# Optimization experiments

Measured on AMD Instinct MI355X. Metric: run time of the kernel, lower is better.

Reference implementation:

```python
import jax, jax.numpy as jnp
import numpy as np
import math

# Fixed rendering constants (from module-level source)
FOV_X = 60.0
FOV_Y = 60.0
NEAR = 0.1
FAR = 10000.0
SCALE_MODIFIER = 1.0
MAX_FREQUENCY = 128.0
NUM_TOTAL_FREQUENCIES = 1024
GAUSSIAN_ONLY = False
COV_DILATION = 0.3  # low-pass dilation as in 3DGS EWA splatting

N_PRIM = 512
TOP_K = 8
IMG_H = 200
IMG_W = 200


def _quat_to_rotmat(q):
    # q: [N,4] (r, x, y, z), normalized
    q = q / (jnp.linalg.norm(q, axis=-1, keepdims=True) + 1e-8)
    r, x, y, z = q[:, 0], q[:, 1], q[:, 2], q[:, 3]
    R = jnp.stack([
        jnp.stack([1 - 2 * (y * y + z * z), 2 * (x * y - r * z), 2 * (x * z + r * y)], -1),
        jnp.stack([2 * (x * y + r * z), 1 - 2 * (x * x + z * z), 2 * (y * z - r * x)], -1),
        jnp.stack([2 * (x * z - r * y), 2 * (y * z + r * x), 1 - 2 * (x * x + y * y)], -1),
    ], axis=-2)  # [N,3,3]
    return R


def _forward(colors, opacities, background_color, positions, scales, rotations,
             topk_wave_coefficients, topk_wave_indices, cam_position,
             view_matrix, VP_matrix, image_width, image_height):
    H, W = image_height, image_width
    N = positions.shape[0]
    tan_x = math.tan(math.radians(FOV_X * 0.5))
    tan_y = math.tan(math.radians(FOV_Y * 0.5))
    fx = W / (2.0 * tan_x)
    fy = H / (2.0 * tan_y)

    # --- 3D covariance: Sigma = R diag(s^2) R^T, s = exp(log_scales) * modifier
    R = _quat_to_rotmat(rotations)                     # [N,3,3]
    s = jnp.exp(scales) * SCALE_MODIFIER               # [N,3]
    Sigma = jnp.einsum('nij,nj,nkj->nik', R, s * s, R)  # [N,3,3]

    # --- projection
    p_hom = jnp.concatenate([positions, jnp.ones((N, 1), positions.dtype)], -1)  # [N,4]
    t_cam = jnp.einsum('ij,nj->ni', view_matrix, p_hom)[:, :3]                   # [N,3] camera space
    clip = jnp.einsum('ij,nj->ni', VP_matrix, p_hom)                             # [N,4]
    wclip = clip[:, 3:4]
    ndc = clip[:, :2] / jnp.where(jnp.abs(wclip) > 1e-6, wclip, 1e-6)
    px = (ndc * 0.5 + 0.5) * jnp.array([W, H], positions.dtype)                  # [N,2] pixel center
    depth = t_cam[:, 2]

    # --- EWA 2D covariance: cov2d = J Wr Sigma Wr^T J^T + dilation
    tz = jnp.maximum(depth, NEAR)
    tx, ty = t_cam[:, 0], t_cam[:, 1]
    zeros = jnp.zeros_like(tz)
    J = jnp.stack([
        jnp.stack([fx / tz, zeros, -fx * tx / (tz * tz)], -1),
        jnp.stack([zeros, fy / tz, -fy * ty / (tz * tz)], -1),
    ], axis=-2)                                         # [N,2,3]
    Wr = view_matrix[:3, :3]
    M = jnp.einsum('nij,jk->nik', J, Wr)                # [N,2,3]
    cov2d = jnp.einsum('nab,nbc,ndc->nad', M, Sigma, M) # [N,2,2]
    A = cov2d[:, 0, 0] + COV_DILATION
    B = cov2d[:, 0, 1]
    C = cov2d[:, 1, 1] + COV_DILATION
    det = jnp.maximum(A * C - B * B, 1e-12)
    conA, conB, conC = C / det, -B / det, A / det       # conic (inverse cov)

    # --- pixel grid [H*W]
    ys = jnp.arange(H, dtype=positions.dtype) + 0.5
    xs = jnp.arange(W, dtype=positions.dtype) + 0.5
    gy, gx = jnp.meshgrid(ys, xs, indexing='ij')
    gx, gy = gx.ravel(), gy.ravel()

    dx = px[:, 0:1] - gx[None, :]                       # [N,HW]
    dy = px[:, 1:2] - gy[None, :]
    power = -0.5 * (conA[:, None] * dx * dx + conC[:, None] * dy * dy) - conB[:, None] * dx * dy
    G = jnp.exp(jnp.minimum(power, 0.0))                # [N,HW]

    # --- periodic (Gabor) modulation along projected primary axis of each primitive
    if GAUSSIAN_ONLY:
        wave = 1.0
    else:
        a3 = R[:, :, 0]                                  # local first axis, world space [N,3]
        a2 = jnp.einsum('nij,nj->ni', M, a3)             # projected to screen [N,2]
        a2 = a2 / (jnp.linalg.norm(a2, axis=-1, keepdims=True) + 1e-8)
        tcoord = (dx * a2[:, 0:1] + dy * a2[:, 1:2]) / W  # [N,HW], normalized coord
        freqs = topk_wave_indices.astype(positions.dtype) * (MAX_FREQUENCY / NUM_TOTAL_FREQUENCIES)  # [N,K]
        wave = jnp.zeros_like(tcoord)
        for k in range(topk_wave_indices.shape[1]):      # small fixed K, unrolled
            wave = wave + topk_wave_coefficients[:, k:k + 1] * jnp.cos(
                2.0 * jnp.pi * freqs[:, k:k + 1] * tcoord)

    alpha = jnp.clip(opacities * G * wave, 0.0, 0.99)   # [N,HW]
    valid = (depth > NEAR) & (wclip[:, 0] > 1e-4)
    alpha = jnp.where(valid[:, None], alpha, 0.0)

    # --- depth sort + front-to-back alpha compositing
    order = jnp.argsort(depth)
    alpha_s = alpha[order]
    colors_s = colors[order]
    Tprod = jnp.cumprod(1.0 - alpha_s, axis=0)           # inclusive transmittance
    T_excl = jnp.concatenate([jnp.ones((1, alpha_s.shape[1]), alpha_s.dtype), Tprod[:-1]], 0)
    img = jnp.einsum('nc,np->cp', colors_s, alpha_s * T_excl)  # [3,HW]
    img = img + background_color[:, None] * Tprod[-1][None, :]
    return img.reshape(3, H, W)


def setup_inputs() -> dict:
    key = jax.random.key(0)
    ks = jax.random.split(key, 10)
    N, K = N_PRIM, TOP_K
    colors = jax.random.uniform(ks[0], (N, 3), jnp.float32)
    opacities = 0.8 * jax.random.uniform(ks[1], (N, 1), jnp.float32)
    background_color = jnp.zeros((3,), jnp.float32)
    # positions inside the view frustum: z in [4,12], xy in [-3,3]
    xy = jax.random.uniform(ks[2], (N, 2), jnp.float32, -3.0, 3.0)
    z = jax.random.uniform(ks[3], (N, 1), jnp.float32, 4.0, 12.0)
    positions = jnp.concatenate([xy, z], -1)
    scales = -2.5 + 0.3 * jax.random.normal(ks[4], (N, 3), jnp.float32)  # log-scales
    rotations = jax.random.normal(ks[5], (N, 4), jnp.float32)
    topk_wave_coefficients = 0.1 * jax.random.normal(ks[6], (N, K), jnp.float32)
    topk_wave_indices = jax.random.randint(ks[7], (N, K), 1, NUM_TOTAL_FREQUENCIES).astype(jnp.int32)
    cam_position = jnp.zeros((3,), jnp.float32)
    view_matrix = jnp.eye(4, dtype=jnp.float32)
    tan_x = math.tan(math.radians(FOV_X * 0.5))
    tan_y = math.tan(math.radians(FOV_Y * 0.5))
    P = jnp.array([[1.0 / tan_x, 0, 0, 0],
                   [0, 1.0 / tan_y, 0, 0],
                   [0, 0, FAR / (FAR - NEAR), -FAR * NEAR / (FAR - NEAR)],
                   [0, 0, 1.0, 0]], jnp.float32)
    VP_matrix = P @ view_matrix
    return {
        'colors': colors, 'opacities': opacities, 'background_color': background_color,
        'positions': positions, 'scales': scales, 'rotations': rotations,
        'topk_wave_coefficients': topk_wave_coefficients, 'topk_wave_indices': topk_wave_indices,
        'cam_position': cam_position, 'view_matrix': view_matrix, 'VP_matrix': VP_matrix,
        'image_width': IMG_W, 'image_height': IMG_H,
    }


def reference(colors, opacities, background_color, positions, scales, rotations,
              topk_wave_coefficients, topk_wave_indices, cam_position,
              view_matrix, VP_matrix, image_width, image_height):
    return _forward(colors, opacities, background_color, positions, scales, rotations,
                    topk_wave_coefficients, topk_wave_indices, cam_position,
                    view_matrix, VP_matrix, image_width, image_height)
```

## Files before the change

kernel.cpp:

```cpp
#include <hip/hip_runtime.h>
#include <math.h>

#define NPRIM   512
#define TOPK    8
#define PSTRIDE 28
#define IMG     200
#define NPIX    (IMG * IMG)
#define NSEG    8
#define SEGSZ   (NPRIM / NSEG)
#define TILE    64
#define TILES_X (IMG / 8)


__global__ __launch_bounds__(NPRIM) void prep_kernel(
    const float* __restrict__ colors,
    const float* __restrict__ opacities,
    const float* __restrict__ positions,
    const float* __restrict__ scales,
    const float* __restrict__ rotations,
    const float* __restrict__ wcoef,
    const int*   __restrict__ widx,
    const float* __restrict__ view,
    const float* __restrict__ VP,
    float* __restrict__ table,
    float4* __restrict__ bbox)
{
    const int n = threadIdx.x;
    const float tanx = 0.57735026918962576451f;
    const float fx = IMG / (2.0f * tanx);
    const float fy = IMG / (2.0f * tanx);

    float qr = rotations[n*4+0], qx = rotations[n*4+1];
    float qy = rotations[n*4+2], qz = rotations[n*4+3];
    float qn = sqrtf(qr*qr + qx*qx + qy*qy + qz*qz) + 1e-8f;
    qr /= qn; qx /= qn; qy /= qn; qz /= qn;
    float R00 = 1.f - 2.f*(qy*qy + qz*qz), R01 = 2.f*(qx*qy - qr*qz), R02 = 2.f*(qx*qz + qr*qy);
    float R10 = 2.f*(qx*qy + qr*qz), R11 = 1.f - 2.f*(qx*qx + qz*qz), R12 = 2.f*(qy*qz - qr*qx);
    float R20 = 2.f*(qx*qz - qr*qy), R21 = 2.f*(qy*qz + qr*qx), R22 = 1.f - 2.f*(qx*qx + qy*qy);

    float s0 = expf(scales[n*3+0]); s0 *= s0;
    float s1 = expf(scales[n*3+1]); s1 *= s1;
    float s2 = expf(scales[n*3+2]); s2 *= s2;

    float S00 = R00*R00*s0 + R01*R01*s1 + R02*R02*s2;
    float S01 = R00*R10*s0 + R01*R11*s1 + R02*R12*s2;
    float S02 = R00*R20*s0 + R01*R21*s1 + R02*R22*s2;
    float S11 = R10*R10*s0 + R11*R11*s1 + R12*R12*s2;
    float S12 = R10*R20*s0 + R11*R21*s1 + R12*R22*s2;
    float S22 = R20*R20*s0 + R21*R21*s1 + R22*R22*s2;

    float px_ = positions[n*3+0], py_ = positions[n*3+1], pz_ = positions[n*3+2];
    float t0 = view[0]*px_ + view[1]*py_ + view[2]*pz_  + view[3];
    float t1 = view[4]*px_ + view[5]*py_ + view[6]*pz_  + view[7];
    float t2 = view[8]*px_ + view[9]*py_ + view[10]*pz_ + view[11];
    float c0 = VP[0]*px_  + VP[1]*py_  + VP[2]*pz_  + VP[3];
    float c1 = VP[4]*px_  + VP[5]*py_  + VP[6]*pz_  + VP[7];
    float w  = VP[12]*px_ + VP[13]*py_ + VP[14]*pz_ + VP[15];

    float denom = (fabsf(w) > 1e-6f) ? w : 1e-6f;
    float pxs = (c0/denom * 0.5f + 0.5f) * (float)IMG;
    float pys = (c1/denom * 0.5f + 0.5f) * (float)IMG;

    float depth = t2;
    float tz = fmaxf(depth, 0.1f);
    float invz = 1.f / tz;
    float J00 = fx*invz, J02 = -fx*t0*invz*invz;
    float J11 = fy*invz, J12 = -fy*t1*invz*invz;

    float M00 = J00*view[0] + J02*view[8];
    float M01 = J00*view[1] + J02*view[9];
    float M02 = J00*view[2] + J02*view[10];
    float M10 = J11*view[4] + J12*view[8];
    float M11 = J11*view[5] + J12*view[9];
    float M12 = J11*view[6] + J12*view[10];

    float T00 = M00*S00 + M01*S01 + M02*S02;
    float T01 = M00*S01 + M01*S11 + M02*S12;
    float T02 = M00*S02 + M01*S12 + M02*S22;
    float T10 = M10*S00 + M11*S01 + M12*S02;
    float T11 = M10*S01 + M11*S11 + M12*S12;
    float T12 = M10*S02 + M11*S12 + M12*S22;
    float cA = T00*M00 + T01*M01 + T02*M02 + 0.3f;
    float cB = T00*M10 + T01*M11 + T02*M12;
    float cC = T10*M10 + T11*M11 + T12*M12 + 0.3f;
    float det  = fmaxf(cA*cC - cB*cB, 1e-12f);
    float idet = 1.f / det;
    float conA = cC*idet, conB = -cB*idet, conC = cA*idet;

    float a2x = M00*R00 + M01*R10 + M02*R20;
    float a2y = M10*R00 + M11*R10 + M12*R20;
    float an = sqrtf(a2x*a2x + a2y*a2y) + 1e-8f;
    a2x = (a2x/an) * (1.0f/(float)IMG);
    a2y = (a2y/an) * (1.0f/(float)IMG);

    bool valid = (depth > 0.1f) && (w > 1e-4f);
    float op = valid ? opacities[n] : 0.0f;

    float rx = valid ? sqrtf(fmaxf(30.f * cA, 0.f)) : -1e30f;
    float ry = valid ? sqrtf(fmaxf(30.f * cC, 0.f)) : -1e30f;

    __shared__ float sd[NPRIM];
    sd[n] = depth;
    __syncthreads();
    int rank = 0;
#pragma unroll 8
    for (int m = 0; m < NPRIM; ++m) {
        float dm = sd[m];
        rank += (dm < depth) || (dm == depth && m < n);
    }

    float* e = table + rank * PSTRIDE;
    e[0]=pxs; e[1]=pys; e[2]=conA; e[3]=conB; e[4]=conC;
    e[5]=a2x; e[6]=a2y; e[7]=op;
    e[8]=colors[n*3+0]; e[9]=colors[n*3+1]; e[10]=colors[n*3+2]; e[11]=0.f;
#pragma unroll
    for (int k = 0; k < TOPK; ++k) {
        e[12+k] = wcoef[n*TOPK+k];
        e[20+k] = 0.78539816339744830962f * (float)widx[n*TOPK+k];
    }
    bbox[rank] = make_float4(pxs, pys, rx, ry);
}

__global__ __launch_bounds__(NSEG*64, 4) void render_kernel(
    const float*  __restrict__ table,
    const float4* __restrict__ bbox,
    const float*  __restrict__ bg,
    float* __restrict__ out)
{
    __shared__ float  lds[NPRIM * PSTRIDE];
    __shared__ float4 part[NSEG * TILE];

    const int lane = threadIdx.x & 63;
    const int wv   = threadIdx.x >> 6;
    const int tx   = blockIdx.x % TILES_X, ty = blockIdx.x / TILES_X;
    const int x    = tx*8 + (lane & 7);
    const int y    = ty*8 + (lane >> 3);
    const float gx = (float)x + 0.5f, gy = (float)y + 0.5f;

    {
        const float4* src = (const float4*)table + wv * (SEGSZ * PSTRIDE / 4);
        float4*       dst = (float4*)lds         + wv * (SEGSZ * PSTRIDE / 4);
#pragma unroll
        for (int q = 0; q < 7; ++q) dst[q*64 + lane] = src[q*64 + lane];
    }

    const float tcx = (float)(tx*8) + 4.0f, tcy = (float)(ty*8) + 4.0f;
    float4 bb = bbox[wv * SEGSZ + lane];
    bool active = (fabsf(bb.x - tcx) <= bb.z + 3.5f) &&
                  (fabsf(bb.y - tcy) <= bb.w + 3.5f);
    unsigned long long mask = __ballot(active);

    float T = 1.f, cr = 0.f, cg = 0.f, cb = 0.f;
    const float* seg = lds + (wv * SEGSZ) * PSTRIDE;
    while (mask) {
        int j = __ffsll((unsigned long long)mask) - 1;
        mask &= mask - 1;
        const float* h = seg + j * PSTRIDE;
        float4 q0 = *(const float4*)(h);
        float4 q1 = *(const float4*)(h + 4);
        float dx = q0.x - gx, dy = q0.y - gy;
        float pw = -0.5f*(q0.z*dx*dx + q1.x*dy*dy) - q0.w*dx*dy;
        if (__any(pw > -15.0f)) {
            float4 q2 = *(const float4*)(h + 8);
            float4 c0 = *(const float4*)(h + 12), c1 = *(const float4*)(h + 16);
            float4 w0 = *(const float4*)(h + 20), w1 = *(const float4*)(h + 24);
            float G = __expf(fminf(pw, 0.f));
            float t = dx*q1.y + dy*q1.z;
            float wave = c0.x*__cosf(w0.x*t) + c0.y*__cosf(w0.y*t)
                       + c0.z*__cosf(w0.z*t) + c0.w*__cosf(w0.w*t)
                       + c1.x*__cosf(w1.x*t) + c1.y*__cosf(w1.y*t)
                       + c1.z*__cosf(w1.z*t) + c1.w*__cosf(w1.w*t);
            float a = fminf(fmaxf(q1.w * G * wave, 0.f), 0.99f);
            float wgt = a * T;
            cr += q2.x*wgt; cg += q2.y*wgt; cb += q2.z*wgt;
            T *= (1.f - a);
        }
    }
    part[wv*TILE + lane] = make_float4(cr, cg, cb, T);

    __syncthreads();

    if (threadIdx.x < TILE) {
        float Ta = 1.f, fr = 0.f, fg = 0.f, fb = 0.f;
#pragma unroll
        for (int s = 0; s < NSEG; ++s) {
            float4 v = part[s*TILE + lane];
            fr += Ta * v.x; fg += Ta * v.y; fb += Ta * v.z;
            Ta *= v.w;
        }
        const int p = y*IMG + x;
        out[p]          = fr + bg[0]*Ta;
        out[NPIX + p]   = fg + bg[1]*Ta;
        out[2*NPIX + p] = fb + bg[2]*Ta;
    }
}

extern "C" void kernel_launch(void* const* d_in, const int* in_sizes, int n_in,
                              void* d_out, int out_size, void* d_ws, size_t ws_size,
                              hipStream_t stream) {
    const float* colors  = (const float*)d_in[0];
    const float* opac    = (const float*)d_in[1];
    const float* bg      = (const float*)d_in[2];
    const float* pos     = (const float*)d_in[3];
    const float* scales  = (const float*)d_in[4];
    const float* rot     = (const float*)d_in[5];
    const float* wcoef   = (const float*)d_in[6];
    const int*   widx    = (const int*)d_in[7];
    const float* view    = (const float*)d_in[9];
    const float* VP      = (const float*)d_in[10];

    float*  table = (float*)d_ws;
    float4* bbox  = (float4*)((char*)d_ws + NPRIM * PSTRIDE * sizeof(float));

    hipLaunchKernelGGL(prep_kernel, dim3(1), dim3(NPRIM), 0, stream,
                       colors, opac, pos, scales, rot, wcoef, widx, view, VP,
                       table, bbox);
    hipLaunchKernelGGL(render_kernel, dim3(TILES_X*TILES_X), dim3(NSEG*64), 0, stream,
                       table, bbox, bg, (float*)d_out);
}
```

Measured before the change: 95.01 us.

## Split prep across blocks and read primitive table directly from global memory

The prep kernel now runs as eight 64-thread blocks. Each block recomputes every primitive's depth into shared memory so it can rank its own primitives, and the rank loop reads depths four at a time. The render kernel drops the 57 KB shared-memory staging of the primitive table and reads it from global/cache with a wave-uniform index via readfirstlane, which frees LDS for occupancy and removes the copy. The cost is per-primitive loads that may go through the vector cache rather than LDS, and redundant depth computation in every prep block.

Result: slower. 98.73 us (+3.9%).

```diff
diff --git a/kernel.cpp b/kernel.cpp
--- a/kernel.cpp
+++ b/kernel.cpp
@@ -12,7 +12,7 @@
 #define TILES_X (IMG / 8)
 
 
-__global__ __launch_bounds__(NPRIM) void prep_kernel(
+__global__ __launch_bounds__(64) void prep_kernel(
     const float* __restrict__ colors,
     const float* __restrict__ opacities,
     const float* __restrict__ positions,
@@ -25,7 +25,18 @@
     float* __restrict__ table,
     float4* __restrict__ bbox)
 {
-    const int n = threadIdx.x;
+    __shared__ float sd[NPRIM];
+    const int lane = threadIdx.x;
+    const int n    = blockIdx.x * 64 + lane;
+
+    const float v8 = view[8], v9 = view[9], v10 = view[10], v11 = view[11];
+#pragma unroll
+    for (int k = 0; k < 8; ++k) {
+        int m = k * 64 + lane;
+        sd[m] = v8*positions[m*3+0] + v9*positions[m*3+1] + v10*positions[m*3+2] + v11;
+    }
+    __syncthreads();
+
     const float tanx = 0.57735026918962576451f;
     const float fx = IMG / (2.0f * tanx);
     const float fy = IMG / (2.0f * tanx);
@@ -52,7 +63,7 @@
     float px_ = positions[n*3+0], py_ = positions[n*3+1], pz_ = positions[n*3+2];
     float t0 = view[0]*px_ + view[1]*py_ + view[2]*pz_  + view[3];
     float t1 = view[4]*px_ + view[5]*py_ + view[6]*pz_  + view[7];
-    float t2 = view[8]*px_ + view[9]*py_ + view[10]*pz_ + view[11];
+    float depth = sd[n];
     float c0 = VP[0]*px_  + VP[1]*py_  + VP[2]*pz_  + VP[3];
     float c1 = VP[4]*px_  + VP[5]*py_  + VP[6]*pz_  + VP[7];
     float w  = VP[12]*px_ + VP[13]*py_ + VP[14]*pz_ + VP[15];
@@ -61,7 +72,6 @@
     float pxs = (c0/denom * 0.5f + 0.5f) * (float)IMG;
     float pys = (c1/denom * 0.5f + 0.5f) * (float)IMG;
 
-    float depth = t2;
     float tz = fmaxf(depth, 0.1f);
     float invz = 1.f / tz;
     float J00 = fx*invz, J02 = -fx*t0*invz*invz;
@@ -99,14 +109,14 @@
     float rx = valid ? sqrtf(fmaxf(30.f * cA, 0.f)) : -1e30f;
     float ry = valid ? sqrtf(fmaxf(30.f * cC, 0.f)) : -1e30f;
 
-    __shared__ float sd[NPRIM];
-    sd[n] = depth;
-    __syncthreads();
     int rank = 0;
-#pragma unroll 8
-    for (int m = 0; m < NPRIM; ++m) {
-        float dm = sd[m];
-        rank += (dm < depth) || (dm == depth && m < n);
+#pragma unroll 4
+    for (int m = 0; m < NPRIM; m += 4) {
+        float4 d4 = *(const float4*)(sd + m);
+        rank += (d4.x < depth) || (d4.x == depth && (m+0) < n);
+        rank += (d4.y < depth) || (d4.y == depth && (m+1) < n);
+        rank += (d4.z < depth) || (d4.z == depth && (m+2) < n);
+        rank += (d4.w < depth) || (d4.w == depth && (m+3) < n);
     }
 
     float* e = table + rank * PSTRIDE;
@@ -121,13 +131,12 @@
     bbox[rank] = make_float4(pxs, pys, rx, ry);
 }
 
-__global__ __launch_bounds__(NSEG*64, 4) void render_kernel(
+__global__ __launch_bounds__(NSEG*64) void render_kernel(
     const float*  __restrict__ table,
     const float4* __restrict__ bbox,
     const float*  __restrict__ bg,
     float* __restrict__ out)
 {
-    __shared__ float  lds[NPRIM * PSTRIDE];
     __shared__ float4 part[NSEG * TILE];
 
     const int lane = threadIdx.x & 63;
@@ -137,13 +146,6 @@
     const int y    = ty*8 + (lane >> 3);
     const float gx = (float)x + 0.5f, gy = (float)y + 0.5f;
 
-    {
-        const float4* src = (const float4*)table + wv * (SEGSZ * PSTRIDE / 4);
-        float4*       dst = (float4*)lds         + wv * (SEGSZ * PSTRIDE / 4);
-#pragma unroll
-        for (int q = 0; q < 7; ++q) dst[q*64 + lane] = src[q*64 + lane];
-    }
-
     const float tcx = (float)(tx*8) + 4.0f, tcy = (float)(ty*8) + 4.0f;
     float4 bb = bbox[wv * SEGSZ + lane];
     bool active = (fabsf(bb.x - tcx) <= bb.z + 3.5f) &&
@@ -151,10 +153,11 @@
     unsigned long long mask = __ballot(active);
 
     float T = 1.f, cr = 0.f, cg = 0.f, cb = 0.f;
-    const float* seg = lds + (wv * SEGSZ) * PSTRIDE;
+    const float* seg = table + (wv * SEGSZ) * PSTRIDE;
     while (mask) {
-        int j = __ffsll((unsigned long long)mask) - 1;
+        int j = __ffsll(mask) - 1;
         mask &= mask - 1;
+        j = __builtin_amdgcn_readfirstlane(j);
         const float* h = seg + j * PSTRIDE;
         float4 q0 = *(const float4*)(h);
         float4 q1 = *(const float4*)(h + 4);
@@ -212,7 +215,7 @@
     float*  table = (float*)d_ws;
     float4* bbox  = (float4*)((char*)d_ws + NPRIM * PSTRIDE * sizeof(float));
 
-    hipLaunchKernelGGL(prep_kernel, dim3(1), dim3(NPRIM), 0, stream,
+    hipLaunchKernelGGL(prep_kernel, dim3(NPRIM/64), dim3(64), 0, stream,
                        colors, opac, pos, scales, rot, wcoef, widx, view, VP,
                        table, bbox);
     hipLaunchKernelGGL(render_kernel, dim3(TILES_X*TILES_X), dim3(NSEG*64), 0, stream,
```
